# Kernel tuning notes

Hardware: AMD Instinct MI355X
Metric: run time of the kernel (lower is better)

Reference implementation:

```python
import jax, jax.numpy as jnp
import numpy as np

ALPHA = 0.25          # VQLayer commitment weight
KL_WEIGHT = 0.01      # settings.kl_weight (repo global)
ENTROPY_WEIGHT = 0.1  # settings.entropy_weight (repo global)


def _forward(x, W0, b0, W1, b1, Wmu, bmu, Wvar, bvar, protos, eps):
    # MLP encoder: input_dim -> 64 -> output_dim, relu after each layer
    h = jax.nn.relu(x @ W0.T + b0)
    h = jax.nn.relu(h @ W1.T + b1)
    logvar = h @ Wvar.T + bvar
    mu = h @ Wmu.T + bmu
    # reparameterize
    latents = mu + eps * jnp.exp(0.5 * logvar)  # [B, D]

    # squared euclidean distances to prototypes: [B, P]
    dists = (jnp.sum(latents ** 2, axis=1, keepdims=True)
             + jnp.sum(protos ** 2, axis=1)
             - 2.0 * latents @ protos.T)
    idx = jnp.argmin(dists, axis=1)              # [B]
    quantized = protos[idx]                      # == one_hot @ protos

    commitment_loss = jnp.mean((jax.lax.stop_gradient(quantized) - latents) ** 2)
    embedding_loss = jnp.mean((quantized - jax.lax.stop_gradient(latents)) ** 2)
    vq_loss = commitment_loss * ALPHA + embedding_loss

    # categorical entropy of mean soft assignment
    logdist = jax.nn.log_softmax(-dists, axis=1)
    soft_dist = jnp.mean(jnp.exp(logdist), axis=0) + 1e-6
    soft_dist = soft_dist / jnp.sum(soft_dist)
    ent = jnp.sum(-soft_dist * jnp.log(soft_dist))
    vq_loss = vq_loss + ENTROPY_WEIGHT * ent

    # straight-through estimator
    quantized = latents + jax.lax.stop_gradient(quantized - latents)

    divergence = jnp.mean(-0.5 * jnp.sum(1.0 + logvar - mu ** 2 - jnp.exp(logvar), axis=1))
    total_loss = KL_WEIGHT * divergence + vq_loss
    return quantized, total_loss, divergence


def setup_inputs() -> dict:
    key = jax.random.key(0)
    ks = jax.random.split(key, 12)
    B, IN, HID, D, P = 32768, 1024, 64, 512, 2048

    def lin(k, fan_in, fan_out):
        bound = 1.0 / np.sqrt(fan_in)
        k1, k2 = jax.random.split(k)
        W = jax.random.uniform(k1, (fan_out, fan_in), jnp.float32, -bound, bound)
        b = jax.random.uniform(k2, (fan_out,), jnp.float32, -bound, bound)
        return W, b

    W0, b0 = lin(ks[0], IN, HID)
    W1, b1 = lin(ks[1], HID, D)
    Wmu, bmu = lin(ks[2], D, D)
    Wvar, bvar = lin(ks[3], D, D)
    protos = jax.random.uniform(ks[4], (P, D), jnp.float32, -1.0 / P, 1.0 / P)
    x = jax.random.normal(ks[5], (B, IN), jnp.float32)
    eps = jax.random.normal(ks[6], (B, D), jnp.float32)
    return {"x": x, "W0": W0, "b0": b0, "W1": W1, "b1": b1,
            "Wmu": Wmu, "bmu": bmu, "Wvar": Wvar, "bvar": bvar,
            "protos": protos, "eps": eps}


def reference(x, W0, b0, W1, b1, Wmu, bmu, Wvar, bvar, protos, eps):
    return _forward(x, W0, b0, W1, b1, Wmu, bmu, Wvar, bvar, protos, eps)
```

## Files before the change

### kernel.cpp

```cpp
#include <hip/hip_runtime.h>
#include <math.h>

#define B_N 32768
#define IN_DIM 1024
#define HID 64
#define D_DIM 512
#define P_N 2048

typedef __attribute__((ext_vector_type(8))) short s16x8;
typedef __attribute__((ext_vector_type(4))) float f32x4;

__device__ __forceinline__ unsigned short f2bf(float f) {
    unsigned u = __float_as_uint(f);
    return (unsigned short)((u + 0x7fffu + ((u >> 16) & 1u)) >> 16);
}
__device__ __forceinline__ float bf2f(unsigned short v) {
    return __uint_as_float(((unsigned)v) << 16);
}

__device__ __forceinline__ void gl_lds(const void* gsrc, void* ldst) {
    __builtin_amdgcn_global_load_lds(
        (const __attribute__((address_space(1))) unsigned int*)gsrc,
        (__attribute__((address_space(3))) unsigned int*)ldst, 16, 0, 0);
}

__global__ __launch_bounds__(256) void k_pack(const float* __restrict__ src,
                                              unsigned short* __restrict__ dst,
                                              int nrows, int nk8) {
    int gid = blockIdx.x * 256 + threadIdx.x;
    if (gid >= nrows * nk8) return;
    int row = gid / nk8, k8 = gid % nk8;
    int K32 = k8 >> 2;
    int lane = (row & 15) | ((k8 & 3) << 4);
    int P16 = row >> 4;
    int nk32 = nk8 >> 2;
    const float* s = src + (size_t)row * (nk8 * 8) + k8 * 8;
    float4 x = *(const float4*)s;
    float4 y = *(const float4*)(s + 4);
    s16x8 o;
    o[0] = (short)f2bf(x.x); o[1] = (short)f2bf(x.y);
    o[2] = (short)f2bf(x.z); o[3] = (short)f2bf(x.w);
    o[4] = (short)f2bf(y.x); o[5] = (short)f2bf(y.y);
    o[6] = (short)f2bf(y.z); o[7] = (short)f2bf(y.w);
    ((s16x8*)dst)[((size_t)P16 * nk32 + K32) * 64 + lane] = o;
}

__global__ __launch_bounds__(256) void k_packrm(const float* __restrict__ src,
                                                unsigned short* __restrict__ dst,
                                                int nrows) {
    int gid = blockIdx.x * 256 + threadIdx.x;
    if (gid >= nrows * 64) return;
    int row = gid >> 6, k8 = gid & 63;
    const float* s = src + (size_t)row * 512 + k8 * 8;
    float4 x = *(const float4*)s;
    float4 y = *(const float4*)(s + 4);
    s16x8 o;
    o[0] = (short)f2bf(x.x); o[1] = (short)f2bf(x.y);
    o[2] = (short)f2bf(x.z); o[3] = (short)f2bf(x.w);
    o[4] = (short)f2bf(y.x); o[5] = (short)f2bf(y.y);
    o[6] = (short)f2bf(y.z); o[7] = (short)f2bf(y.w);
    ((s16x8*)(dst))[(size_t)row * 64 + k8] = o;
}

__global__ __launch_bounds__(256) void k_packmv(const float* __restrict__ Wmu,
                                                const float* __restrict__ Wvar,
                                                unsigned short* __restrict__ dst) {
    int gid = blockIdx.x * 256 + threadIdx.x;
    int row = gid >> 6, k8 = gid & 63;
    int g = row >> 5, i = row & 31;
    const float* s = (i < 16 ? Wmu + (size_t)(g * 16 + i) * 512
                             : Wvar + (size_t)(g * 16 + i - 16) * 512) + k8 * 8;
    float4 x = *(const float4*)s;
    float4 y = *(const float4*)(s + 4);
    s16x8 o;
    o[0] = (short)f2bf(x.x); o[1] = (short)f2bf(x.y);
    o[2] = (short)f2bf(x.z); o[3] = (short)f2bf(x.w);
    o[4] = (short)f2bf(y.x); o[5] = (short)f2bf(y.y);
    o[6] = (short)f2bf(y.z); o[7] = (short)f2bf(y.w);
    ((s16x8*)(dst))[(size_t)row * 64 + k8] = o;
}

__global__ __launch_bounds__(256, 4) void k_enc1(const float* __restrict__ x,
                                                 const unsigned short* __restrict__ w0p,
                                                 const float* __restrict__ b0,
                                                 unsigned short* __restrict__ h1b) {
    __shared__ s16x8 As[2048];
    const int tid = threadIdx.x;
    const int l = tid & 63, wid = tid >> 6;
    const int bm = blockIdx.x * 128;
    const s16x8* w0p8 = (const s16x8*)w0p;

    const int srow = tid >> 1, ssub = tid & 1;
    const int srb = srow * 256, ssw = (srow & 7) << 4;

    const int klane = (l >> 4) << 4;
    const int sw = (l & 7) << 4;
    int aoff[2];
#pragma unroll
    for (int m = 0; m < 2; ++m) aoff[m] = (wid * 32 + m * 16 + (l & 15)) * 256;

    f32x4 acc[2][4];
#pragma unroll
    for (int m = 0; m < 2; ++m)
#pragma unroll
        for (int pf = 0; pf < 4; ++pf) acc[m][pf] = (f32x4)0.f;

    for (int kt = 0; kt < 8; ++kt) {
        const float* src = x + (size_t)(bm + srow) * IN_DIM + kt * 128 + ssub * 64;
#pragma unroll
        for (int it = 0; it < 8; ++it) {
            float4 a = *(const float4*)(src + it * 8);
            float4 b = *(const float4*)(src + it * 8 + 4);
            s16x8 o;
            o[0] = (short)f2bf(a.x); o[1] = (short)f2bf(a.y);
            o[2] = (short)f2bf(a.z); o[3] = (short)f2bf(a.w);
            o[4] = (short)f2bf(b.x); o[5] = (short)f2bf(b.y);
            o[6] = (short)f2bf(b.z); o[7] = (short)f2bf(b.w);
            int kbyte = ssub * 128 + it * 16;
            As[(srb + (kbyte ^ ssw)) >> 4] = o;
        }
        __syncthreads();
#pragma unroll
        for (int K32 = 0; K32 < 4; ++K32) {
            const int Kg = kt * 4 + K32;
            s16x8 b[4];
#pragma unroll
            for (int pf = 0; pf < 4; ++pf) b[pf] = w0p8[((size_t)pf * 32 + Kg) * 64 + l];
            const int kb = (K32 * 64 + klane) ^ sw;
            s16x8 a[2];
#pragma unroll
            for (int m = 0; m < 2; ++m) a[m] = As[(aoff[m] + kb) >> 4];
#pragma unroll
            for (int m = 0; m < 2; ++m)
#pragma unroll
                for (int pf = 0; pf < 4; ++pf)
                    acc[m][pf] = __builtin_amdgcn_mfma_f32_16x16x32_bf16(a[m], b[pf], acc[m][pf], 0, 0, 0);
        }
        __syncthreads();
    }
#pragma unroll
    for (int m = 0; m < 2; ++m)
#pragma unroll
        for (int pf = 0; pf < 4; ++pf) {
            const int c = pf * 16 + (l & 15);
            const float bb = b0[c];
#pragma unroll
            for (int j = 0; j < 4; ++j) {
                const int r = bm + wid * 32 + m * 16 + (l >> 4) * 4 + j;
                h1b[(size_t)r * HID + c] = f2bf(fmaxf(acc[m][pf][j] + bb, 0.f));
            }
        }
}

__global__ __launch_bounds__(256, 4) void k_enc2(const unsigned short* __restrict__ h1b,
                                                 const unsigned short* __restrict__ w1p,
                                                 const float* __restrict__ b1,
                                                 unsigned short* __restrict__ h2b) {
    __shared__ s16x8 As[512];
    const int tid = threadIdx.x;
    const int l = tid & 63, wid = tid >> 6;
    const int bm = blockIdx.x * 64;
    const s16x8* w1p8 = (const s16x8*)w1p;

#pragma unroll
    for (int it = 0; it < 2; ++it) {
        int g = tid * 2 + it;
        int row = g >> 3, k8 = g & 7;
        s16x8 v = ((const s16x8*)(h1b + (size_t)(bm + row) * HID))[k8];
        As[(row * 128 + ((k8 * 16) ^ ((row & 7) << 4))) >> 4] = v;
    }
    __syncthreads();

    const int arow = wid * 16 + (l & 15);
    const int sw = (l & 7) << 4;
    const int klane = (l >> 4) << 4;
    s16x8 a[2];
#pragma unroll
    for (int K32 = 0; K32 < 2; ++K32)
        a[K32] = As[(arow * 128 + ((K32 * 64 + klane) ^ sw)) >> 4];

    const int r0 = bm + wid * 16 + (l >> 4) * 4;
#pragma unroll
    for (int ct = 0; ct < 4; ++ct) {
        f32x4 acc[8];
#pragma unroll
        for (int pf = 0; pf < 8; ++pf) acc[pf] = (f32x4)0.f;
#pragma unroll
        for (int K32 = 0; K32 < 2; ++K32)
#pragma unroll
            for (int pf = 0; pf < 8; ++pf) {
                s16x8 b = w1p8[(((size_t)(ct * 8 + pf)) * 2 + K32) * 64 + l];
                acc[pf] = __builtin_amdgcn_mfma_f32_16x16x32_bf16(a[K32], b, acc[pf], 0, 0, 0);
            }
#pragma unroll
        for (int pf = 0; pf < 8; ++pf) {
            const int c = ct * 128 + pf * 16 + (l & 15);
            const float bb = b1[c];
#pragma unroll
            for (int j = 0; j < 4; ++j)
                h2b[(size_t)(r0 + j) * D_DIM + c] = f2bf(fmaxf(acc[pf][j] + bb, 0.f));
        }
    }
}

#define GEMM_CORE(Aptr, Bptr)                                                  \
    __shared__ s16x8 A8[1024];                                                 \
    __shared__ s16x8 B8[1024];                                                 \
    const int tid = threadIdx.x;                                               \
    const int l = tid & 63, w = tid >> 6;                                      \
    const int bm = blockIdx.x * 128;                                           \
    const int bn = blockIdx.y * 128;                                           \
    const int wr = w >> 1, wc = w & 1;                                         \
    const int srow = l >> 3;                                                   \
    const int scol = (((l & 7) ^ ((l >> 3) & 7)) * 8);                         \
    f32x4 acc[4][4];                                                           \
    _Pragma("unroll") for (int m = 0; m < 4; ++m)                              \
        _Pragma("unroll") for (int n = 0; n < 4; ++n) acc[m][n] = (f32x4)0.f;  \
    for (int kt = 0; kt < 8; ++kt) {                                           \
        __syncthreads();                                                       \
        _Pragma("unroll") for (int i = 0; i < 4; ++i) {                        \
            const int rb = w * 32 + i * 8;                                     \
            gl_lds(Aptr + (size_t)(bm + rb + srow) * 512 + kt * 64 + scol,     \
                   (char*)A8 + rb * 128);                                      \
            gl_lds(Bptr + (size_t)(bn + rb + srow) * 512 + kt * 64 + scol,     \
                   (char*)B8 + rb * 128);                                      \
        }                                                                      \
        __syncthreads();                                                       \
        _Pragma("unroll") for (int K32 = 0; K32 < 2; ++K32) {                  \
            const int kb = (K32 * 64 + (l >> 4) * 16) ^ ((l & 7) << 4);        \
            s16x8 a[4], b[4];                                                  \
            _Pragma("unroll") for (int m = 0; m < 4; ++m)                      \
                a[m] = A8[((wr * 64 + m * 16 + (l & 15)) * 128 + kb) >> 4];    \
            _Pragma("unroll") for (int n = 0; n < 4; ++n)                      \
                b[n] = B8[((wc * 64 + n * 16 + (l & 15)) * 128 + kb) >> 4];    \
            _Pragma("unroll") for (int m = 0; m < 4; ++m)                      \
                _Pragma("unroll") for (int n = 0; n < 4; ++n)                  \
                    acc[m][n] = __builtin_amdgcn_mfma_f32_16x16x32_bf16(       \
                        a[m], b[n], acc[m][n], 0, 0, 0);                       \
        }                                                                      \
    }

__global__ __launch_bounds__(256, 4) void k_mv(const unsigned short* __restrict__ h2b,
                                               const unsigned short* __restrict__ wmv16,
                                               const float* __restrict__ bmu,
                                               const float* __restrict__ bvar,
                                               const float* __restrict__ eps,
                                               unsigned short* __restrict__ lat16,
                                               float* __restrict__ div_acc) {
    GEMM_CORE(h2b, wmv16)
    __shared__ float red[4];
    float kl = 0.f;
    const int dbase0 = (bn >> 1) + wc * 32;
#pragma unroll
    for (int m = 0; m < 4; ++m)
#pragma unroll
        for (int nn = 0; nn < 2; ++nn) {
            const int d = dbase0 + nn * 16 + (l & 15);
            const float bmv = bmu[d], bvv = bvar[d];
#pragma unroll
            for (int j = 0; j < 4; ++j) {
                const int r = bm + wr * 64 + m * 16 + (l >> 4) * 4 + j;
                float mu = acc[m][2 * nn][j] + bmv;
                float lv = acc[m][2 * nn + 1][j] + bvv;
                float la = fmaf(eps[(size_t)r * D_DIM + d], __expf(0.5f * lv), mu);
                lat16[(size_t)r * D_DIM + d] = f2bf(la);
                kl += mu * mu + __expf(lv) - lv - 1.f;
            }
        }
    kl *= 0.5f;
#pragma unroll
    for (int d = 1; d < 64; d <<= 1) kl += __shfl_xor(kl, d);
    if (l == 0) red[w] = kl;
    __syncthreads();
    if (tid == 0) atomicAdd(div_acc, red[0] + red[1] + red[2] + red[3]);
}

__global__ __launch_bounds__(256) void k_pnorm(const float* __restrict__ protos,
                                               float* __restrict__ pnorm) {
    const int p = blockIdx.x * 4 + (threadIdx.x >> 6);
    const int lane = threadIdx.x & 63;
    const float* row = protos + (size_t)p * D_DIM;
    float4 v1 = *(const float4*)(row + lane * 8);
    float4 v2 = *(const float4*)(row + lane * 8 + 4);
    float s = v1.x * v1.x + v1.y * v1.y + v1.z * v1.z + v1.w * v1.w +
              v2.x * v2.x + v2.y * v2.y + v2.z * v2.z + v2.w * v2.w;
#pragma unroll
    for (int m = 1; m < 64; m <<= 1) s += __shfl_xor(s, m);
    if (lane == 0) pnorm[p] = s;
}

__global__ __launch_bounds__(256, 4) void k_vq1(const unsigned short* __restrict__ lat16,
                                                const unsigned short* __restrict__ pb16,
                                                const float* __restrict__ pnorm,
                                                float* __restrict__ rowS,
                                                unsigned* __restrict__ rowKey,
                                                unsigned short* __restrict__ gA,
                                                unsigned short* __restrict__ gB) {
    GEMM_CORE(lat16, pb16)
    float pn[4];
#pragma unroll
    for (int n = 0; n < 4; ++n) pn[n] = pnorm[bn + wc * 64 + n * 16 + (l & 15)];
    s16x8* gd8 = (s16x8*)((blockIdx.y < 8) ? gA : gB);
    const size_t gbase = ((size_t)((blockIdx.y & 7) * 256 + blockIdx.x) * 8) * 256;
#pragma unroll
    for (int m = 0; m < 4; ++m) {
        float gv[4][4], ev[4][4];
#pragma unroll
        for (int n = 0; n < 4; ++n)
#pragma unroll
            for (int j = 0; j < 4; ++j) {
                gv[n][j] = 2.f * acc[m][n][j] - pn[n];
                ev[n][j] = __expf(gv[n][j]);
            }
        s16x8 u0, u1;
#pragma unroll
        for (int j = 0; j < 4; ++j) {
            u0[j] = (short)f2bf(ev[0][j]); u0[4 + j] = (short)f2bf(ev[1][j]);
            u1[j] = (short)f2bf(ev[2][j]); u1[4 + j] = (short)f2bf(ev[3][j]);
        }
        gd8[gbase + (size_t)(m * 2 + 0) * 256 + tid] = u0;
        gd8[gbase + (size_t)(m * 2 + 1) * 256 + tid] = u1;
#pragma unroll
        for (int j = 0; j < 4; ++j) {
            float se = ev[0][j] + ev[1][j] + ev[2][j] + ev[3][j];
            unsigned key = 0u;
#pragma unroll
            for (int n = 0; n < 4; ++n) {
                const int p = bn + wc * 64 + n * 16 + (l & 15);
                unsigned kk = (__float_as_uint(gv[n][j] + 16.0f) & 0xFFFFF800u) | (unsigned)(2047 - p);
                key = key > kk ? key : kk;
            }
#pragma unroll
            for (int d = 1; d < 16; d <<= 1) {
                se += __shfl_xor(se, d);
                unsigned ok = (unsigned)__shfl_xor((int)key, d);
                key = key > ok ? key : ok;
            }
            if ((l & 15) == 0) {
                const int row = bm + wr * 64 + m * 16 + (l >> 4) * 4 + j;
                atomicAdd(&rowS[row], se);
                atomicMax(&rowKey[row], key);
            }
        }
    }
}

__global__ __launch_bounds__(256, 4) void k_vq2s(const unsigned short* __restrict__ gA,
                                                 const unsigned short* __restrict__ gB,
                                                 const float* __restrict__ rowS,
                                                 float* __restrict__ soft_acc) {
    __shared__ float soft_l[128];
    const int tid = threadIdx.x;
    const int l = tid & 63, w = tid >> 6;
    const int wr = w >> 1, wc = w & 1;
    const int bm = blockIdx.x * 128;
    const int bn = blockIdx.y * 128;
    if (tid < 128) soft_l[tid] = 0.f;
    __syncthreads();

    const s16x8* gs8 = (const s16x8*)((blockIdx.y < 8) ? gA : gB);
    const size_t gbase = ((size_t)((blockIdx.y & 7) * 256 + blockIdx.x) * 8) * 256;

    float is[4][4];
#pragma unroll
    for (int m = 0; m < 4; ++m)
#pragma unroll
        for (int j = 0; j < 4; ++j)
            is[m][j] = 1.0f / rowS[bm + wr * 64 + m * 16 + (l >> 4) * 4 + j];

    float cs[4] = {0.f, 0.f, 0.f, 0.f};
#pragma unroll
    for (int m = 0; m < 4; ++m) {
        s16x8 u0 = gs8[gbase + (size_t)(m * 2 + 0) * 256 + tid];
        s16x8 u1 = gs8[gbase + (size_t)(m * 2 + 1) * 256 + tid];
#pragma unroll
        for (int j = 0; j < 4; ++j) {
            cs[0] += bf2f((unsigned short)u0[j]) * is[m][j];
            cs[1] += bf2f((unsigned short)u0[4 + j]) * is[m][j];
            cs[2] += bf2f((unsigned short)u1[j]) * is[m][j];
            cs[3] += bf2f((unsigned short)u1[4 + j]) * is[m][j];
        }
    }
#pragma unroll
    for (int n = 0; n < 4; ++n) {
        cs[n] += __shfl_xor(cs[n], 16);
        cs[n] += __shfl_xor(cs[n], 32);
    }
    if (l < 16) {
#pragma unroll
        for (int n = 0; n < 4; ++n) atomicAdd(&soft_l[wc * 64 + n * 16 + l], cs[n]);
    }
    __syncthreads();
    if (tid < 128) atomicAdd(&soft_acc[bn + tid], soft_l[tid]);
}

__global__ __launch_bounds__(256) void k_quant(const float* __restrict__ protos,
                                               const unsigned* __restrict__ rowKey,
                                               const unsigned short* __restrict__ lat16,
                                               float* __restrict__ out,
                                               float* __restrict__ vq_part) {
    const int tid = threadIdx.x;
    const int l = tid & 63, wid = tid >> 6;
    const int base = blockIdx.x * 64;
    float s = 0.f;
#pragma unroll
    for (int it = 0; it < 16; ++it) {
        const int r = base + it * 4 + wid;
        const int p = 2047 - (int)(rowKey[r] & 2047u);
        const float4* qp = (const float4*)(protos + (size_t)p * D_DIM);
        float4* op = (float4*)(out + (size_t)r * D_DIM);
        s16x8 lv = ((const s16x8*)(lat16 + (size_t)r * D_DIM))[l];
        float4 q1 = qp[l * 2], q2 = qp[l * 2 + 1];
        float d0 = q1.x - bf2f((unsigned short)lv[0]);
        float d1 = q1.y - bf2f((unsigned short)lv[1]);
        float d2 = q1.z - bf2f((unsigned short)lv[2]);
        float d3 = q1.w - bf2f((unsigned short)lv[3]);
        float d4 = q2.x - bf2f((unsigned short)lv[4]);
        float d5 = q2.y - bf2f((unsigned short)lv[5]);
        float d6 = q2.z - bf2f((unsigned short)lv[6]);
        float d7 = q2.w - bf2f((unsigned short)lv[7]);
        s += d0 * d0 + d1 * d1 + d2 * d2 + d3 * d3 +
             d4 * d4 + d5 * d5 + d6 * d6 + d7 * d7;
        op[l * 2] = q1; op[l * 2 + 1] = q2;
    }
#pragma unroll
    for (int m = 1; m < 64; m <<= 1) s += __shfl_xor(s, m);
    __shared__ float red[4];
    if (l == 0) red[wid] = s;
    __syncthreads();
    if (tid == 0) vq_part[blockIdx.x] = red[0] + red[1] + red[2] + red[3];
}

__global__ __launch_bounds__(256) void k_final(const float* __restrict__ soft_acc,
                                               const float* __restrict__ scal,
                                               const float* __restrict__ vq_part,
                                               float* __restrict__ out) {
    const int tid = threadIdx.x;
    __shared__ float red[256];
    float vals[8];
    float s = 0.f;
#pragma unroll
    for (int i = 0; i < 8; ++i) {
        float v = soft_acc[tid * 8 + i] * (1.0f / B_N) + 1e-6f;
        vals[i] = v;
        s += v;
    }
    red[tid] = s;
    __syncthreads();
    for (int off = 128; off > 0; off >>= 1) {
        if (tid < off) red[tid] += red[tid + off];
        __syncthreads();
    }
    float norm = red[0];
    __syncthreads();
    float e = 0.f;
#pragma unroll
    for (int i = 0; i < 8; ++i) {
        float p = vals[i] / norm;
        e -= p * __logf(p);
    }
    red[tid] = e;
    __syncthreads();
    for (int off = 128; off > 0; off >>= 1) {
        if (tid < off) red[tid] += red[tid + off];
        __syncthreads();
    }
    float ent = red[0];
    __syncthreads();
    red[tid] = vq_part[tid] + vq_part[tid + 256];
    __syncthreads();
    for (int off = 128; off > 0; off >>= 1) {
        if (tid < off) red[tid] += red[tid + off];
        __syncthreads();
    }
    if (tid == 0) {
        float div = scal[0] * (1.0f / B_N);
        float vq = red[0] * (1.0f / ((float)B_N * (float)D_DIM));
        float vq_loss = 1.25f * vq + 0.1f * ent;
        float total = 0.01f * div + vq_loss;
        out[(size_t)B_N * D_DIM] = total;
        out[(size_t)B_N * D_DIM + 1] = div;
    }
}

extern "C" void kernel_launch(void* const* d_in, const int* in_sizes, int n_in,
                              void* d_out, int out_size, void* d_ws, size_t ws_size,
                              hipStream_t stream) {
    const float* x = (const float*)d_in[0];
    const float* W0 = (const float*)d_in[1];
    const float* b0 = (const float*)d_in[2];
    const float* W1 = (const float*)d_in[3];
    const float* b1 = (const float*)d_in[4];
    const float* Wmu = (const float*)d_in[5];
    const float* bmu = (const float*)d_in[6];
    const float* Wvar = (const float*)d_in[7];
    const float* bvar = (const float*)d_in[8];
    const float* protos = (const float*)d_in[9];
    const float* eps = (const float*)d_in[10];
    float* out = (float*)d_out;

    unsigned short* wsp = (unsigned short*)d_ws;
    unsigned short* lat16 = wsp;
    unsigned short* pb16 = lat16 + (size_t)B_N * D_DIM;
    unsigned short* wmv16 = pb16 + (size_t)P_N * D_DIM;
    unsigned short* w0pack = wmv16 + (size_t)2 * D_DIM * D_DIM;
    unsigned short* w1pack = w0pack + (size_t)HID * IN_DIM;
    float* pnorm = (float*)(w1pack + (size_t)D_DIM * HID);
    float* rowS = pnorm + P_N;
    unsigned* rowKey = (unsigned*)(rowS + B_N);
    float* soft = (float*)(rowKey + B_N);
    float* scal = soft + P_N;
    float* vqpart = scal + 2;
    unsigned short* h1b = (unsigned short*)(vqpart + 512);
    unsigned short* h2b = h1b + (size_t)B_N * HID;
    unsigned short* gA = h1b;
    unsigned short* gB = (unsigned short*)d_out;

    hipMemsetAsync(rowS, 0, (size_t)(B_N * 2 + P_N + 2) * 4, stream);

    k_pack<<<(HID * (IN_DIM / 8) + 255) / 256, 256, 0, stream>>>(W0, w0pack, HID, IN_DIM / 8);
    k_pack<<<(D_DIM * (HID / 8) + 255) / 256, 256, 0, stream>>>(W1, w1pack, D_DIM, HID / 8);
    k_packrm<<<P_N * 64 / 256, 256, 0, stream>>>(protos, pb16, P_N);
    k_packmv<<<1024 * 64 / 256, 256, 0, stream>>>(Wmu, Wvar, wmv16);
    k_pnorm<<<P_N / 4, 256, 0, stream>>>(protos, pnorm);

    k_enc1<<<B_N / 128, 256, 0, stream>>>(x, w0pack, b0, h1b);
    k_enc2<<<B_N / 64, 256, 0, stream>>>(h1b, w1pack, b1, h2b);

    dim3 gmv(B_N / 128, 8);
    k_mv<<<gmv, 256, 0, stream>>>(h2b, wmv16, bmu, bvar, eps, lat16, scal);

    dim3 gvq(B_N / 128, 16);
    k_vq1<<<gvq, 256, 0, stream>>>(lat16, pb16, pnorm, rowS, rowKey, gA, gB);
    k_vq2s<<<gvq, 256, 0, stream>>>(gA, gB, rowS, soft);

    k_quant<<<B_N / 64, 256, 0, stream>>>(protos, rowKey, lat16, out, vqpart);
    k_final<<<1, 256, 0, stream>>>(soft, scal, vqpart, out);
}
```

Measured before the change: 316.0 us.

## Merge prep kernels and swizzle GEMM block order for XCD L2 locality

Five small packing and norm kernels become a single k_prep launch, which removes launch overhead. k_mv and k_vq1 now use 1D grids whose block index is remapped with a stride of 8, so that blocks sent round-robin to the same XCD share A and B tiles in that XCD's L2. The remapping also changes which blocks run together, which could change how the two operands' reuse balances across the XCDs.

```diff
diff --git a/kernel.cpp b/kernel.cpp
--- a/kernel.cpp
+++ b/kernel.cpp
@@ -24,17 +24,7 @@
         (__attribute__((address_space(3))) unsigned int*)ldst, 16, 0, 0);
 }
 
-__global__ __launch_bounds__(256) void k_pack(const float* __restrict__ src,
-                                              unsigned short* __restrict__ dst,
-                                              int nrows, int nk8) {
-    int gid = blockIdx.x * 256 + threadIdx.x;
-    if (gid >= nrows * nk8) return;
-    int row = gid / nk8, k8 = gid % nk8;
-    int K32 = k8 >> 2;
-    int lane = (row & 15) | ((k8 & 3) << 4);
-    int P16 = row >> 4;
-    int nk32 = nk8 >> 2;
-    const float* s = src + (size_t)row * (nk8 * 8) + k8 * 8;
+__device__ __forceinline__ s16x8 pack8(const float* s) {
     float4 x = *(const float4*)s;
     float4 y = *(const float4*)(s + 4);
     s16x8 o;
@@ -42,42 +32,58 @@
     o[2] = (short)f2bf(x.z); o[3] = (short)f2bf(x.w);
     o[4] = (short)f2bf(y.x); o[5] = (short)f2bf(y.y);
     o[6] = (short)f2bf(y.z); o[7] = (short)f2bf(y.w);
-    ((s16x8*)dst)[((size_t)P16 * nk32 + K32) * 64 + lane] = o;
-}
-
-__global__ __launch_bounds__(256) void k_packrm(const float* __restrict__ src,
-                                                unsigned short* __restrict__ dst,
-                                                int nrows) {
+    return o;
+}
+
+__global__ __launch_bounds__(256) void k_prep(const float* __restrict__ protos,
+                                              const float* __restrict__ Wmu,
+                                              const float* __restrict__ Wvar,
+                                              const float* __restrict__ W0,
+                                              const float* __restrict__ W1,
+                                              unsigned short* __restrict__ pb16,
+                                              float* __restrict__ pnorm,
+                                              unsigned short* __restrict__ wmv16,
+                                              unsigned short* __restrict__ w0pack,
+                                              unsigned short* __restrict__ w1pack) {
     int gid = blockIdx.x * 256 + threadIdx.x;
-    if (gid >= nrows * 64) return;
-    int row = gid >> 6, k8 = gid & 63;
-    const float* s = src + (size_t)row * 512 + k8 * 8;
-    float4 x = *(const float4*)s;
-    float4 y = *(const float4*)(s + 4);
-    s16x8 o;
-    o[0] = (short)f2bf(x.x); o[1] = (short)f2bf(x.y);
-    o[2] = (short)f2bf(x.z); o[3] = (short)f2bf(x.w);
-    o[4] = (short)f2bf(y.x); o[5] = (short)f2bf(y.y);
-    o[6] = (short)f2bf(y.z); o[7] = (short)f2bf(y.w);
-    ((s16x8*)(dst))[(size_t)row * 64 + k8] = o;
-}
-
-__global__ __launch_bounds__(256) void k_packmv(const float* __restrict__ Wmu,
-                                                const float* __restrict__ Wvar,
-                                                unsigned short* __restrict__ dst) {
-    int gid = blockIdx.x * 256 + threadIdx.x;
-    int row = gid >> 6, k8 = gid & 63;
-    int g = row >> 5, i = row & 31;
-    const float* s = (i < 16 ? Wmu + (size_t)(g * 16 + i) * 512
-                             : Wvar + (size_t)(g * 16 + i - 16) * 512) + k8 * 8;
-    float4 x = *(const float4*)s;
-    float4 y = *(const float4*)(s + 4);
-    s16x8 o;
-    o[0] = (short)f2bf(x.x); o[1] = (short)f2bf(x.y);
-    o[2] = (short)f2bf(x.z); o[3] = (short)f2bf(x.w);
-    o[4] = (short)f2bf(y.x); o[5] = (short)f2bf(y.y);
-    o[6] = (short)f2bf(y.z); o[7] = (short)f2bf(y.w);
-    ((s16x8*)(dst))[(size_t)row * 64 + k8] = o;
+    if (gid < 131072) {
+        int row = gid >> 6, k8 = gid & 63;
+        const float* s = protos + (size_t)row * 512 + k8 * 8;
+        float4 x = *(const float4*)s;
+        float4 y = *(const float4*)(s + 4);
+        s16x8 o;
+        o[0] = (short)f2bf(x.x); o[1] = (short)f2bf(x.y);
+        o[2] = (short)f2bf(x.z); o[3] = (short)f2bf(x.w);
+        o[4] = (short)f2bf(y.x); o[5] = (short)f2bf(y.y);
+        o[6] = (short)f2bf(y.z); o[7] = (short)f2bf(y.w);
+        ((s16x8*)pb16)[(size_t)row * 64 + k8] = o;
+        float ss = x.x * x.x + x.y * x.y + x.z * x.z + x.w * x.w +
+                   y.x * y.x + y.y * y.y + y.z * y.z + y.w * y.w;
+#pragma unroll
+        for (int d = 1; d < 64; d <<= 1) ss += __shfl_xor(ss, d);
+        if ((threadIdx.x & 63) == 0) pnorm[row] = ss;
+    } else if (gid < 196608) {
+        int a = gid - 131072;
+        int row = a >> 6, k8 = a & 63;
+        int g = row >> 5, i = row & 31;
+        const float* s = (i < 16 ? Wmu + (size_t)(g * 16 + i) * 512
+                                 : Wvar + (size_t)(g * 16 + i - 16) * 512) + k8 * 8;
+        ((s16x8*)wmv16)[(size_t)row * 64 + k8] = pack8(s);
+    } else if (gid < 204800) {
+        int a = gid - 196608;
+        int row = a >> 7, k8 = a & 127;
+        int K32 = k8 >> 2;
+        int lane = (row & 15) | ((k8 & 3) << 4);
+        ((s16x8*)w0pack)[((size_t)(row >> 4) * 32 + K32) * 64 + lane] =
+            pack8(W0 + (size_t)row * IN_DIM + k8 * 8);
+    } else {
+        int a = gid - 204800;
+        int row = a >> 3, k8 = a & 7;
+        int K32 = k8 >> 2;
+        int lane = (row & 15) | ((k8 & 3) << 4);
+        ((s16x8*)w1pack)[((size_t)(row >> 4) * 2 + K32) * 64 + lane] =
+            pack8(W1 + (size_t)row * HID + k8 * 8);
+    }
 }
 
 __global__ __launch_bounds__(256, 4) void k_enc1(const float* __restrict__ x,
@@ -109,13 +115,7 @@
         const float* src = x + (size_t)(bm + srow) * IN_DIM + kt * 128 + ssub * 64;
 #pragma unroll
         for (int it = 0; it < 8; ++it) {
-            float4 a = *(const float4*)(src + it * 8);
-            float4 b = *(const float4*)(src + it * 8 + 4);
-            s16x8 o;
-            o[0] = (short)f2bf(a.x); o[1] = (short)f2bf(a.y);
-            o[2] = (short)f2bf(a.z); o[3] = (short)f2bf(a.w);
-            o[4] = (short)f2bf(b.x); o[5] = (short)f2bf(b.y);
-            o[6] = (short)f2bf(b.z); o[7] = (short)f2bf(b.w);
+            s16x8 o = pack8(src + it * 8);
             int kbyte = ssub * 128 + it * 16;
             As[(srb + (kbyte ^ ssw)) >> 4] = o;
         }
@@ -203,13 +203,13 @@
     }
 }
 
-#define GEMM_CORE(Aptr, Bptr)                                                  \
+#define GEMM_CORE(Aptr, Bptr, BME, BNE)                                        \
     __shared__ s16x8 A8[1024];                                                 \
     __shared__ s16x8 B8[1024];                                                 \
     const int tid = threadIdx.x;                                               \
     const int l = tid & 63, w = tid >> 6;                                      \
-    const int bm = blockIdx.x * 128;                                           \
-    const int bn = blockIdx.y * 128;                                           \
+    const int bm = (BME);                                                      \
+    const int bn = (BNE);                                                      \
     const int wr = w >> 1, wc = w & 1;                                         \
     const int srow = l >> 3;                                                   \
     const int scol = (((l & 7) ^ ((l >> 3) & 7)) * 8);                         \
@@ -247,7 +247,8 @@
                                                const float* __restrict__ eps,
                                                unsigned short* __restrict__ lat16,
                                                float* __restrict__ div_acc) {
-    GEMM_CORE(h2b, wmv16)
+    const int bswz = (blockIdx.x & 7) * 256 + (blockIdx.x >> 3);
+    GEMM_CORE(h2b, wmv16, (bswz >> 3) * 128, (bswz & 7) * 128)
     __shared__ float red[4];
     float kl = 0.f;
     const int dbase0 = (bn >> 1) + wc * 32;
@@ -275,20 +276,6 @@
     if (tid == 0) atomicAdd(div_acc, red[0] + red[1] + red[2] + red[3]);
 }
 
-__global__ __launch_bounds__(256) void k_pnorm(const float* __restrict__ protos,
-                                               float* __restrict__ pnorm) {
-    const int p = blockIdx.x * 4 + (threadIdx.x >> 6);
-    const int lane = threadIdx.x & 63;
-    const float* row = protos + (size_t)p * D_DIM;
-    float4 v1 = *(const float4*)(row + lane * 8);
-    float4 v2 = *(const float4*)(row + lane * 8 + 4);
-    float s = v1.x * v1.x + v1.y * v1.y + v1.z * v1.z + v1.w * v1.w +
-              v2.x * v2.x + v2.y * v2.y + v2.z * v2.z + v2.w * v2.w;
-#pragma unroll
-    for (int m = 1; m < 64; m <<= 1) s += __shfl_xor(s, m);
-    if (lane == 0) pnorm[p] = s;
-}
-
 __global__ __launch_bounds__(256, 4) void k_vq1(const unsigned short* __restrict__ lat16,
                                                 const unsigned short* __restrict__ pb16,
                                                 const float* __restrict__ pnorm,
@@ -296,12 +283,14 @@
                                                 unsigned* __restrict__ rowKey,
                                                 unsigned short* __restrict__ gA,
                                                 unsigned short* __restrict__ gB) {
-    GEMM_CORE(lat16, pb16)
+    const int bswz = (blockIdx.x & 7) * 512 + (blockIdx.x >> 3);
+    const int bmi = bswz >> 4, bni = bswz & 15;
+    GEMM_CORE(lat16, pb16, bmi * 128, bni * 128)
     float pn[4];
 #pragma unroll
     for (int n = 0; n < 4; ++n) pn[n] = pnorm[bn + wc * 64 + n * 16 + (l & 15)];
-    s16x8* gd8 = (s16x8*)((blockIdx.y < 8) ? gA : gB);
-    const size_t gbase = ((size_t)((blockIdx.y & 7) * 256 + blockIdx.x) * 8) * 256;
+    s16x8* gd8 = (s16x8*)((bni < 8) ? gA : gB);
+    const size_t gbase = ((size_t)((bni & 7) * 256 + bmi) * 8) * 256;
 #pragma unroll
     for (int m = 0; m < 4; ++m) {
         float gv[4][4], ev[4][4];
@@ -518,20 +507,16 @@
 
     hipMemsetAsync(rowS, 0, (size_t)(B_N * 2 + P_N + 2) * 4, stream);
 
-    k_pack<<<(HID * (IN_DIM / 8) + 255) / 256, 256, 0, stream>>>(W0, w0pack, HID, IN_DIM / 8);
-    k_pack<<<(D_DIM * (HID / 8) + 255) / 256, 256, 0, stream>>>(W1, w1pack, D_DIM, HID / 8);
-    k_packrm<<<P_N * 64 / 256, 256, 0, stream>>>(protos, pb16, P_N);
-    k_packmv<<<1024 * 64 / 256, 256, 0, stream>>>(Wmu, Wvar, wmv16);
-    k_pnorm<<<P_N / 4, 256, 0, stream>>>(protos, pnorm);
+    k_prep<<<816, 256, 0, stream>>>(protos, Wmu, Wvar, W0, W1,
+                                    pb16, pnorm, wmv16, w0pack, w1pack);
 
     k_enc1<<<B_N / 128, 256, 0, stream>>>(x, w0pack, b0, h1b);
     k_enc2<<<B_N / 64, 256, 0, stream>>>(h1b, w1pack, b1, h2b);
 
-    dim3 gmv(B_N / 128, 8);
-    k_mv<<<gmv, 256, 0, stream>>>(h2b, wmv16, bmu, bvar, eps, lat16, scal);
-
+    k_mv<<<2048, 256, 0, stream>>>(h2b, wmv16, bmu, bvar, eps, lat16, scal);
+
+    k_vq1<<<4096, 256, 0, stream>>>(lat16, pb16, pnorm, rowS, rowKey, gA, gB);
     dim3 gvq(B_N / 128, 16);
-    k_vq1<<<gvq, 256, 0, stream>>>(lat16, pb16, pnorm, rowS, rowKey, gA, gB);
     k_vq2s<<<gvq, 256, 0, stream>>>(gA, gB, rowS, soft);
 
     k_quant<<<B_N / 64, 256, 0, stream>>>(protos, rowKey, lat16, out, vqpart);
```

New measurement: 375.4 us. +18.8%, slower.
